# Kernel optimization log

Hardware: AMD Instinct MI355X
Metric: run time of the kernel (lower is better)

The kernel has to match this reference:

```python
import jax, jax.numpy as jnp
import numpy as np

B, S, D = 2, 2048, 1024
H, HD = 16, 64


def setup_inputs() -> dict:
    key = jax.random.key(0)
    ks = jax.random.split(key, 6)
    hidden_states = jax.random.normal(ks[0], (B, S, D), dtype=jnp.float32)
    c_attn_w = jax.random.normal(ks[1], (D, 3 * D), dtype=jnp.float32) * 0.02
    c_attn_b = jnp.zeros((3 * D,), dtype=jnp.float32)
    c_proj_w = jax.random.normal(ks[2], (D, D), dtype=jnp.float32) * 0.02
    c_proj_b = jnp.zeros((D,), dtype=jnp.float32)
    basis = jax.random.normal(ks[3], (H, HD, HD), dtype=jnp.float32) * 0.1
    projectors = jnp.einsum('hdr,her->hde', basis, basis)  # basis @ basis.T per head
    return {
        'hidden_states': hidden_states,
        'c_attn_w': c_attn_w,
        'c_attn_b': c_attn_b,
        'c_proj_w': c_proj_w,
        'c_proj_b': c_proj_b,
        'projectors': projectors,
    }


def reference(hidden_states, c_attn_w, c_attn_b, c_proj_w, c_proj_b, projectors):
    # GPT2 Conv1D: out = x @ W + b
    qkv = hidden_states @ c_attn_w + c_attn_b  # [B,S,3D]
    q, k, v = jnp.split(qkv, 3, axis=-1)
    # split heads -> [B,H,S,HD]
    def split_heads(t):
        return t.reshape(B, S, H, HD).transpose(0, 2, 1, 3)
    q, k, v = split_heads(q), split_heads(k), split_heads(v)
    scores = jnp.einsum('bhqd,bhkd->bhqk', q, k) / jnp.sqrt(jnp.float32(HD))
    causal = jnp.tril(jnp.ones((S, S), dtype=bool))
    scores = jnp.where(causal, scores, jnp.finfo(scores.dtype).min)
    probs = jax.nn.softmax(scores, axis=-1)
    attn = jnp.einsum('bhqk,bhkd->bhqd', probs, v)  # [B,H,S,HD]
    # per-head basis projector applied to attention output
    attn = jnp.einsum('bhsd,hde->bhse', attn, projectors)
    # merge heads -> [B,S,D]
    attn = attn.transpose(0, 2, 1, 3).reshape(B, S, D)
    out = attn @ c_proj_w + c_proj_b
    return out
```

## Files before the change

kernel.cpp:

```cpp
#include <hip/hip_runtime.h>

typedef __attribute__((ext_vector_type(8))) short bhalf8;
typedef __attribute__((ext_vector_type(4))) float f32x4;
typedef __attribute__((ext_vector_type(8))) unsigned short u16x8;
typedef __attribute__((ext_vector_type(4))) unsigned short u16x4;

#define BDIM 2
#define SDIM 2048
#define DDIM 1024
#define HDIM 16
#define HDHD 64

__device__ __forceinline__ unsigned short f2bf(float f) {
  unsigned u = __builtin_bit_cast(unsigned, f);
  u += 0x7fffu + ((u >> 16) & 1u);
  return (unsigned short)(u >> 16);
}

__global__ __launch_bounds__(256) void cvt_hidden(const float* __restrict__ x,
                                                  unsigned short* __restrict__ y) {
  size_t i = ((size_t)blockIdx.x * 256 + threadIdx.x) * 4;
  f32x4 v = *(const f32x4*)(x + i);
  u16x4 o;
  o[0] = f2bf(v[0]); o[1] = f2bf(v[1]); o[2] = f2bf(v[2]); o[3] = f2bf(v[3]);
  *(u16x4*)(y + i) = o;
}

__global__ __launch_bounds__(256) void transpose_cvt(const float* __restrict__ W,
                                                     unsigned short* __restrict__ Wt,
                                                     int R, int C) {
  __shared__ float tl[32][33];
  int rt = blockIdx.x * 32, ct = blockIdx.y * 32;
  int r8 = threadIdx.x >> 5, c = threadIdx.x & 31;
#pragma unroll
  for (int i = 0; i < 4; i++)
    tl[r8 + i * 8][c] = W[(size_t)(rt + r8 + i * 8) * C + ct + c];
  __syncthreads();
#pragma unroll
  for (int i = 0; i < 4; i++)
    Wt[(size_t)(ct + r8 + i * 8) * R + rt + c] = f2bf(tl[c][r8 + i * 8]);
}

__global__ __launch_bounds__(256) void make_wproj(const float* __restrict__ proj,
                                                  const float* __restrict__ wproj,
                                                  unsigned short* __restrict__ WT) {
  int h = blockIdx.x, ot = blockIdx.y * 64;
  __shared__ float Pl[64][65];
  __shared__ float Wl[64][65];
  int t = threadIdx.x;
#pragma unroll
  for (int i = 0; i < 16; i++) {
    int idx = t + 256 * i;
    int a = idx >> 6, bc = idx & 63;
    Pl[a][bc] = proj[(size_t)h * 4096 + idx];
    Wl[a][bc] = wproj[(size_t)(h * 64 + a) * 1024 + ot + bc];
  }
  __syncthreads();
  int d = t & 63, ob = t >> 6;
#pragma unroll
  for (int i = 0; i < 16; i++) {
    int o = ob + i * 4;
    float acc = 0.f;
#pragma unroll
    for (int e = 0; e < 64; e++) acc += Pl[d][e] * Wl[e][o];
    WT[(size_t)(ot + o) * 1024 + h * 64 + d] = f2bf(acc);
  }
}

template <int EPI>
__global__ __launch_bounds__(256) void gemm_bt(
    const unsigned short* __restrict__ A, const unsigned short* __restrict__ Bt,
    const float* __restrict__ bias, float* __restrict__ Cf,
    unsigned short* __restrict__ q, unsigned short* __restrict__ k,
    unsigned short* __restrict__ v, int M, int N, int K) {
  __shared__ unsigned short As[128][72];
  __shared__ unsigned short Bs[128][72];
  const int tid = threadIdx.x;
  const int m0 = blockIdx.y * 128, n0 = blockIdx.x * 128;
  f32x4 acc[4][4];
#pragma unroll
  for (int m = 0; m < 4; m++)
#pragma unroll
    for (int n = 0; n < 4; n++) acc[m][n] = f32x4{0.f, 0.f, 0.f, 0.f};
  const int w = tid >> 6, lane = tid & 63;
  const int wr = (w >> 1) * 64, wc = (w & 1) * 64;
  const int lrow = lane & 15, lk = (lane >> 4) * 8;

  for (int kt = 0; kt < K; kt += 64) {
    __syncthreads();
#pragma unroll
    for (int i = 0; i < 4; i++) {
      int cch = tid + 256 * i;
      int r = cch >> 3, c8 = cch & 7;
      *(u16x8*)(&As[r][c8 * 8]) = *(const u16x8*)(A + (size_t)(m0 + r) * K + kt + c8 * 8);
      *(u16x8*)(&Bs[r][c8 * 8]) = *(const u16x8*)(Bt + (size_t)(n0 + r) * K + kt + c8 * 8);
    }
    __syncthreads();
#pragma unroll
    for (int kk = 0; kk < 2; kk++) {
      bhalf8 af[4], bfr[4];
#pragma unroll
      for (int m = 0; m < 4; m++) af[m] = *(const bhalf8*)(&As[wr + m * 16 + lrow][kk * 32 + lk]);
#pragma unroll
      for (int n = 0; n < 4; n++) bfr[n] = *(const bhalf8*)(&Bs[wc + n * 16 + lrow][kk * 32 + lk]);
#pragma unroll
      for (int m = 0; m < 4; m++)
#pragma unroll
        for (int n = 0; n < 4; n++)
          acc[m][n] = __builtin_amdgcn_mfma_f32_16x16x32_bf16(af[m], bfr[n], acc[m][n], 0, 0, 0);
    }
  }
  const int g = lane >> 4, il = lane & 15;
#pragma unroll
  for (int m = 0; m < 4; m++) {
    int rowb = wr + m * 16 + 4 * g;
#pragma unroll
    for (int n = 0; n < 4; n++) {
      int col = n0 + wc + n * 16 + il;
      float bs = bias[col];
#pragma unroll
      for (int r = 0; r < 4; r++) {
        int row = m0 + rowb + r;
        float val = acc[m][n][r] + bs;
        if (EPI == 0) {
          int which = col >> 10, hh = (col >> 6) & 15, hd = col & 63;
          int b = row >> 11, s = row & 2047;
          size_t idx = ((size_t)(b * 16 + hh) * SDIM + s) * HDHD + hd;
          unsigned short bv = f2bf(which == 0 ? val * 0.125f : val);
          if (which == 0) q[idx] = bv;
          else if (which == 1) k[idx] = bv;
          else v[idx] = bv;
        } else {
          Cf[(size_t)row * N + col] = val;
        }
      }
    }
  }
}

__global__ __launch_bounds__(256, 4) void attn_kernel(const unsigned short* __restrict__ Q,
                                                      const unsigned short* __restrict__ Kb,
                                                      const unsigned short* __restrict__ Vb,
                                                      unsigned short* __restrict__ Om) {
  __shared__ unsigned short Ks[64][72];
  __shared__ unsigned short Vt[64][72];
  __shared__ unsigned short Ps[4][16][72];
  const int bh = blockIdx.x;
  const int qt = 31 - blockIdx.y;
  const int tid = threadIdx.x;
  const int w = tid >> 6, lane = tid & 63;
  const int g = lane >> 4, il = lane & 15;
  const int qbase = qt * 64 + w * 16;
  const size_t bhS = (size_t)bh * SDIM;

  bhalf8 qf0, qf1;
  {
    const unsigned short* qp = Q + (bhS + qbase + il) * HDHD + g * 8;
    qf0 = *(const bhalf8*)(qp);
    qf1 = *(const bhalf8*)(qp + 32);
  }
  f32x4 oacc[4];
#pragma unroll
  for (int i = 0; i < 4; i++) oacc[i] = f32x4{0.f, 0.f, 0.f, 0.f};
  float mrun[4], lrun[4];
#pragma unroll
  for (int r = 0; r < 4; r++) { mrun[r] = -1e30f; lrun[r] = 0.f; }

  const int srow = tid >> 2;
  const int schk = (tid & 3) * 16;
  const int nt = qt + 1;

  for (int kt = 0; kt < nt; kt++) {
    const size_t kbase = (bhS + (size_t)kt * 64) * HDHD;
    __syncthreads();
    {
      const unsigned short* src = Kb + kbase + srow * HDHD + schk;
      *(u16x8*)(&Ks[srow][schk]) = *(const u16x8*)(src);
      *(u16x8*)(&Ks[srow][schk + 8]) = *(const u16x8*)(src + 8);
    }
    {
      const unsigned short* vsrc = Vb + kbase + (size_t)(w * 16) * HDHD + lane;
      u16x8 va, vb2;
#pragma unroll
      for (int i = 0; i < 8; i++) va[i] = vsrc[i * HDHD];
#pragma unroll
      for (int i = 0; i < 8; i++) vb2[i] = vsrc[(8 + i) * HDHD];
      *(u16x8*)(&Vt[lane][w * 16]) = va;
      *(u16x8*)(&Vt[lane][w * 16 + 8]) = vb2;
    }
    __syncthreads();
    f32x4 s[4];
#pragma unroll
    for (int c = 0; c < 4; c++) s[c] = f32x4{0.f, 0.f, 0.f, 0.f};
#pragma unroll
    for (int c = 0; c < 4; c++) {
      bhalf8 k0 = *(const bhalf8*)(&Ks[c * 16 + il][g * 8]);
      bhalf8 k1 = *(const bhalf8*)(&Ks[c * 16 + il][32 + g * 8]);
      s[c] = __builtin_amdgcn_mfma_f32_16x16x32_bf16(qf0, k0, s[c], 0, 0, 0);
      s[c] = __builtin_amdgcn_mfma_f32_16x16x32_bf16(qf1, k1, s[c], 0, 0, 0);
    }
    const bool diag = (kt == qt);
    const int kc0 = kt * 64 + il;
#pragma unroll
    for (int r = 0; r < 4; r++) {
      float v0 = s[0][r], v1 = s[1][r], v2 = s[2][r], v3 = s[3][r];
      if (diag) {
        int qr = qbase + 4 * g + r;
        if (kc0 > qr) v0 = -1e30f;
        if (kc0 + 16 > qr) v1 = -1e30f;
        if (kc0 + 32 > qr) v2 = -1e30f;
        if (kc0 + 48 > qr) v3 = -1e30f;
      }
      float mx = fmaxf(fmaxf(v0, v1), fmaxf(v2, v3));
      mx = fmaxf(mx, __shfl_xor(mx, 1));
      mx = fmaxf(mx, __shfl_xor(mx, 2));
      mx = fmaxf(mx, __shfl_xor(mx, 4));
      mx = fmaxf(mx, __shfl_xor(mx, 8));
      float mn = fmaxf(mrun[r], mx);
      float sc = __expf(mrun[r] - mn);
      mrun[r] = mn;
      float p0 = __expf(v0 - mn), p1 = __expf(v1 - mn);
      float p2 = __expf(v2 - mn), p3 = __expf(v3 - mn);
      float rs = p0 + p1 + p2 + p3;
      rs += __shfl_xor(rs, 1);
      rs += __shfl_xor(rs, 2);
      rs += __shfl_xor(rs, 4);
      rs += __shfl_xor(rs, 8);
      lrun[r] = lrun[r] * sc + rs;
      int pr = 4 * g + r;
      Ps[w][pr][il] = f2bf(p0);
      Ps[w][pr][16 + il] = f2bf(p1);
      Ps[w][pr][32 + il] = f2bf(p2);
      Ps[w][pr][48 + il] = f2bf(p3);
#pragma unroll
      for (int df = 0; df < 4; df++) oacc[df][r] *= sc;
    }
#pragma unroll
    for (int kk = 0; kk < 2; kk++) {
      bhalf8 pf = *(const bhalf8*)(&Ps[w][il][kk * 32 + g * 8]);
#pragma unroll
      for (int df = 0; df < 4; df++) {
        bhalf8 vf = *(const bhalf8*)(&Vt[df * 16 + il][kk * 32 + g * 8]);
        oacc[df] = __builtin_amdgcn_mfma_f32_16x16x32_bf16(pf, vf, oacc[df], 0, 0, 0);
      }
    }
  }
  const int b = bh >> 4, h = bh & 15;
#pragma unroll
  for (int r = 0; r < 4; r++) {
    int srow2 = qbase + 4 * g + r;
    float inv = 1.f / lrun[r];
#pragma unroll
    for (int df = 0; df < 4; df++) {
      Om[((size_t)b * SDIM + srow2) * DDIM + h * HDHD + df * 16 + il] =
          f2bf(oacc[df][r] * inv);
    }
  }
}

extern "C" void kernel_launch(void* const* d_in, const int* in_sizes, int n_in,
                              void* d_out, int out_size, void* d_ws, size_t ws_size,
                              hipStream_t stream) {
  const float* hidden = (const float*)d_in[0];
  const float* attn_w = (const float*)d_in[1];
  const float* attn_b = (const float*)d_in[2];
  const float* proj_w = (const float*)d_in[3];
  const float* proj_b = (const float*)d_in[4];
  const float* projectors = (const float*)d_in[5];
  float* out = (float*)d_out;
  char* ws = (char*)d_ws;
  (void)in_sizes; (void)n_in; (void)out_size; (void)ws_size;

  unsigned short* hseq   = (unsigned short*)(ws);
  unsigned short* wqkvT  = (unsigned short*)(ws + 8388608);
  unsigned short* qb     = (unsigned short*)(ws + 14680064);
  unsigned short* kb     = (unsigned short*)(ws + 23068672);
  unsigned short* vb     = (unsigned short*)(ws + 31457280);
  unsigned short* attnM  = (unsigned short*)(ws + 39845888);
  unsigned short* wprojT = (unsigned short*)(ws + 48234496);

  cvt_hidden<<<dim3(4096), dim3(256), 0, stream>>>(hidden, hseq);
  transpose_cvt<<<dim3(32, 96), dim3(256), 0, stream>>>(attn_w, wqkvT, 1024, 3072);
  make_wproj<<<dim3(16, 16), dim3(256), 0, stream>>>(projectors, proj_w, wprojT);
  gemm_bt<0><<<dim3(24, 32), dim3(256), 0, stream>>>(hseq, wqkvT, attn_b, nullptr,
                                                     qb, kb, vb, 4096, 3072, 1024);
  attn_kernel<<<dim3(32, 32), dim3(256), 0, stream>>>(qb, kb, vb, attnM);
  gemm_bt<1><<<dim3(8, 32), dim3(256), 0, stream>>>(attnM, wprojT, proj_b, out,
                                                    nullptr, nullptr, nullptr, 4096, 1024, 1024);
}
```

Measured before the change: 176.9 us.

## Use direct global-to-LDS loads in GEMM and exp2 softmax with conditional rescale

The GEMM tile loads now use global_load_lds to write straight into unpadded LDS, skipping the register round trip. In attention, the log2(e) factor is folded into the Q scale so softmax can call exp2f. The running max and output are rescaled only when the row max grows. s_setprio raises wave priority around the MFMA blocks. The unpadded 64-wide LDS rows may cause bank conflicts on the MFMA fragment reads, and the conditional rescale introduces a branch in the inner loop.

```diff
diff --git a/kernel.cpp b/kernel.cpp
--- a/kernel.cpp
+++ b/kernel.cpp
@@ -10,6 +10,11 @@
 #define DDIM 1024
 #define HDIM 16
 #define HDHD 64
+
+#define GLD16(gaddr, laddr)                                                          \
+  __builtin_amdgcn_global_load_lds(                                                  \
+      (const __attribute__((address_space(1))) unsigned int*)(gaddr),                \
+      (__attribute__((address_space(3))) unsigned int*)(laddr), 16, 0, 0)
 
 __device__ __forceinline__ unsigned short f2bf(float f) {
   unsigned u = __builtin_bit_cast(unsigned, f);
@@ -73,8 +78,8 @@
     const float* __restrict__ bias, float* __restrict__ Cf,
     unsigned short* __restrict__ q, unsigned short* __restrict__ k,
     unsigned short* __restrict__ v, int M, int N, int K) {
-  __shared__ unsigned short As[128][72];
-  __shared__ unsigned short Bs[128][72];
+  __shared__ unsigned short As[128 * 64];
+  __shared__ unsigned short Bs[128 * 64];
   const int tid = threadIdx.x;
   const int m0 = blockIdx.y * 128, n0 = blockIdx.x * 128;
   f32x4 acc[4][4];
@@ -85,24 +90,27 @@
   const int w = tid >> 6, lane = tid & 63;
   const int wr = (w >> 1) * 64, wc = (w & 1) * 64;
   const int lrow = lane & 15, lk = (lane >> 4) * 8;
+  const int srow = tid >> 3, sc8 = (tid & 7) * 8;
 
   for (int kt = 0; kt < K; kt += 64) {
     __syncthreads();
 #pragma unroll
     for (int i = 0; i < 4; i++) {
-      int cch = tid + 256 * i;
-      int r = cch >> 3, c8 = cch & 7;
-      *(u16x8*)(&As[r][c8 * 8]) = *(const u16x8*)(A + (size_t)(m0 + r) * K + kt + c8 * 8);
-      *(u16x8*)(&Bs[r][c8 * 8]) = *(const u16x8*)(Bt + (size_t)(n0 + r) * K + kt + c8 * 8);
+      int c = tid + 256 * i;
+      int r = srow + i * 32;
+      GLD16(A + (size_t)(m0 + r) * K + kt + sc8, As + c * 8);
+      GLD16(Bt + (size_t)(n0 + r) * K + kt + sc8, Bs + c * 8);
     }
     __syncthreads();
 #pragma unroll
     for (int kk = 0; kk < 2; kk++) {
       bhalf8 af[4], bfr[4];
 #pragma unroll
-      for (int m = 0; m < 4; m++) af[m] = *(const bhalf8*)(&As[wr + m * 16 + lrow][kk * 32 + lk]);
-#pragma unroll
-      for (int n = 0; n < 4; n++) bfr[n] = *(const bhalf8*)(&Bs[wc + n * 16 + lrow][kk * 32 + lk]);
+      for (int m = 0; m < 4; m++)
+        af[m] = *(const bhalf8*)(&As[(wr + m * 16 + lrow) * 64 + kk * 32 + lk]);
+#pragma unroll
+      for (int n = 0; n < 4; n++)
+        bfr[n] = *(const bhalf8*)(&Bs[(wc + n * 16 + lrow) * 64 + kk * 32 + lk]);
 #pragma unroll
       for (int m = 0; m < 4; m++)
 #pragma unroll
@@ -126,7 +134,7 @@
           int which = col >> 10, hh = (col >> 6) & 15, hd = col & 63;
           int b = row >> 11, s = row & 2047;
           size_t idx = ((size_t)(b * 16 + hh) * SDIM + s) * HDHD + hd;
-          unsigned short bv = f2bf(which == 0 ? val * 0.125f : val);
+          unsigned short bv = f2bf(which == 0 ? val * 0.1803368801f : val);
           if (which == 0) q[idx] = bv;
           else if (which == 1) k[idx] = bv;
           else v[idx] = bv;
@@ -192,6 +200,7 @@
     f32x4 s[4];
 #pragma unroll
     for (int c = 0; c < 4; c++) s[c] = f32x4{0.f, 0.f, 0.f, 0.f};
+    __builtin_amdgcn_s_setprio(1);
 #pragma unroll
     for (int c = 0; c < 4; c++) {
       bhalf8 k0 = *(const bhalf8*)(&Ks[c * 16 + il][g * 8]);
@@ -199,6 +208,7 @@
       s[c] = __builtin_amdgcn_mfma_f32_16x16x32_bf16(qf0, k0, s[c], 0, 0, 0);
       s[c] = __builtin_amdgcn_mfma_f32_16x16x32_bf16(qf1, k1, s[c], 0, 0, 0);
     }
+    __builtin_amdgcn_s_setprio(0);
     const bool diag = (kt == qt);
     const int kc0 = kt * 64 + il;
 #pragma unroll
@@ -216,25 +226,29 @@
       mx = fmaxf(mx, __shfl_xor(mx, 2));
       mx = fmaxf(mx, __shfl_xor(mx, 4));
       mx = fmaxf(mx, __shfl_xor(mx, 8));
-      float mn = fmaxf(mrun[r], mx);
-      float sc = __expf(mrun[r] - mn);
-      mrun[r] = mn;
-      float p0 = __expf(v0 - mn), p1 = __expf(v1 - mn);
-      float p2 = __expf(v2 - mn), p3 = __expf(v3 - mn);
+      if (mx > mrun[r]) {
+        float sc = exp2f(mrun[r] - mx);
+        mrun[r] = mx;
+        lrun[r] *= sc;
+#pragma unroll
+        for (int df = 0; df < 4; df++) oacc[df][r] *= sc;
+      }
+      float mn = mrun[r];
+      float p0 = exp2f(v0 - mn), p1 = exp2f(v1 - mn);
+      float p2 = exp2f(v2 - mn), p3 = exp2f(v3 - mn);
       float rs = p0 + p1 + p2 + p3;
       rs += __shfl_xor(rs, 1);
       rs += __shfl_xor(rs, 2);
       rs += __shfl_xor(rs, 4);
       rs += __shfl_xor(rs, 8);
-      lrun[r] = lrun[r] * sc + rs;
+      lrun[r] += rs;
       int pr = 4 * g + r;
       Ps[w][pr][il] = f2bf(p0);
       Ps[w][pr][16 + il] = f2bf(p1);
       Ps[w][pr][32 + il] = f2bf(p2);
       Ps[w][pr][48 + il] = f2bf(p3);
-#pragma unroll
-      for (int df = 0; df < 4; df++) oacc[df][r] *= sc;
-    }
+    }
+    __builtin_amdgcn_s_setprio(1);
 #pragma unroll
     for (int kk = 0; kk < 2; kk++) {
       bhalf8 pf = *(const bhalf8*)(&Ps[w][il][kk * 32 + g * 8]);
@@ -244,6 +258,7 @@
         oacc[df] = __builtin_amdgcn_mfma_f32_16x16x32_bf16(pf, vf, oacc[df], 0, 0, 0);
       }
     }
+    __builtin_amdgcn_s_setprio(0);
   }
   const int b = bh >> 4, h = bh & 15;
 #pragma unroll
```

Measured after the change: 197.7 us. 11.7% more time.
